# Kernel tuning notes

Measured on AMD Instinct MI355X. Metric: run time of the kernel, lower is better.

The kernel has to match this reference:

```python
import jax, jax.numpy as jnp
import numpy as np

# Config matching init_kwargs / input_specs
B, H, S, D = 4, 16, 4096, 64
BLK = 16          # sparsity_block
W = 32            # num_local_blocks (banded causal layout: block i attends blocks i-W+1..i)


def setup_inputs() -> dict:
    key = jax.random.key(0)
    kq, kk, kv = jax.random.split(key, 3)
    query = jax.random.normal(kq, (B, H, S, D), dtype=jnp.float16)
    k = jax.random.normal(kk, (B, H, S, D), dtype=jnp.float16)
    value = jax.random.normal(kv, (B, H, S, D), dtype=jnp.float16)
    return {"query": query, "key": k, "value": value}


def reference(query, key, value):
    b, h, s, d = query.shape
    nb = s // BLK
    scale = 1.0 / np.sqrt(d)

    qb = query.reshape(b, h, nb, BLK, d)
    kb = key.reshape(b, h, nb, BLK, d)
    vb = value.reshape(b, h, nb, BLK, d)

    # Banded causal block layout: for query block i, kv block indices i-W+1 .. i
    i = jnp.arange(nb)[:, None]                    # [nb,1]
    w = jnp.arange(W)[None, :]                     # [1,W]
    kv_idx = i - (W - 1) + w                       # [nb,W]
    valid = kv_idx >= 0
    idxc = jnp.clip(kv_idx, 0, nb - 1)

    kg = kb[:, :, idxc]                            # [B,H,nb,W,BLK,D] gathered K blocks
    vg = vb[:, :, idxc]                            # [B,H,nb,W,BLK,D]

    # SDD: block-sparse QK^T, only active blocks are computed
    scores = jnp.einsum('bhnqd,bhnwkd->bhnqwk', qb, kg).astype(jnp.float32) * scale

    # causal + validity mask on global token positions
    q_pos = (jnp.arange(nb) * BLK)[:, None, None, None] + jnp.arange(BLK)[None, :, None, None]  # [nb,BLK,1,1]
    k_pos = (kv_idx * BLK)[:, None, :, None] + jnp.arange(BLK)[None, None, None, :]             # [nb,1,W,BLK]
    mask = (k_pos <= q_pos) & valid[:, None, :, None]
    scores = jnp.where(mask, scores, -jnp.inf)

    # sparse softmax over all active key positions of each query row
    p = jax.nn.softmax(scores.reshape(b, h, nb, BLK, W * BLK), axis=-1)
    p = p.reshape(b, h, nb, BLK, W, BLK).astype(jnp.float16)

    # DSD: sparse-probabilities x dense-V
    out = jnp.einsum('bhnqwk,bhnwkd->bhnqd', p, vg)
    return out.reshape(b, h, s, d)
```

## Files before the change

kernel.cpp:

```cpp
#include <hip/hip_runtime.h>

#define SS 4096
#define DD 64
#define WW 32
#define NEG (-1e30f)
#define CSCALE 0.1803368801f

typedef _Float16 half8_t __attribute__((ext_vector_type(8)));
typedef __fp16 fp16x2_t __attribute__((ext_vector_type(2)));
typedef float float4_t __attribute__((ext_vector_type(4)));

static __device__ __forceinline__ unsigned pk(float a, float b) {
  fp16x2_t h = __builtin_amdgcn_cvt_pkrtz(a, b);
  return __builtin_bit_cast(unsigned, h);
}

static __device__ __forceinline__ half8_t cvt8s(const float* p, float c) {
  float4_t a = *(const float4_t*)p;
  float4_t b = *(const float4_t*)(p + 4);
  union { half8_t h; unsigned u[4]; } x;
  x.u[0] = pk(a[0] * c, a[1] * c);
  x.u[1] = pk(a[2] * c, a[3] * c);
  x.u[2] = pk(b[0] * c, b[1] * c);
  x.u[3] = pk(b[2] * c, b[3] * c);
  return x.h;
}

static __device__ __forceinline__ half8_t lds_frag16(const unsigned short* p) {
  union { half8_t h; uint4 u; } x;
  x.u = *(const uint4*)p;
  return x.h;
}

static __device__ __forceinline__ int ksig(int r) {
  return ((r & 3) ^ ((r >> 3) & 3)) | ((r & 2) << 1);
}

__global__ __launch_bounds__(256, 2)
void sparse_attn_kernel(const float* __restrict__ Q,
                        const float* __restrict__ K,
                        const float* __restrict__ V,
                        float* __restrict__ O) {
  extern __shared__ __align__(16) unsigned short smem[];
  unsigned short* kl = smem;
  unsigned short* vq = smem + 2 * 4096;

  const int lin = blockIdx.x;
  const int xcd = lin & 7;
  const int logical = (lin >> 3) + xcd * ((int)gridDim.x >> 3);
  const int bh = logical >> 5;
  const int i0 = (logical & 31) * 8;

  const int tid = threadIdx.x;
  const int wave = tid >> 6;
  const int lane = tid & 63;
  const int t = lane & 15;
  const int q = lane >> 4;

  const size_t base = (size_t)bh * SS * DD;
  const float* Qb = Q + base;
  const float* Kb = K + base;
  const float* Vb = V + base;

  const int iA = i0 + 2 * wave;
  const int iB = iA + 1;

  const float* qrowA = Qb + (size_t)(iA * 16 + t) * DD;
  const half8_t qfA0 = cvt8s(qrowA + q * 8, CSCALE);
  const half8_t qfA1 = cvt8s(qrowA + 32 + q * 8, CSCALE);
  const float* qrowB = Qb + (size_t)(iB * 16 + t) * DD;
  const half8_t qfB0 = cvt8s(qrowB + q * 8, CSCALE);
  const half8_t qfB1 = cvt8s(qrowB + 32 + q * 8, CSCALE);

  const int prow0 = ((t >> 2) << 3) + (t & 3);
  int koff[2][2];
#pragma unroll
  for (int p = 0; p < 2; ++p)
#pragma unroll
    for (int ro = 0; ro < 2; ++ro) {
      const int rowb = p * 32 + prow0 + ro * 4;
      koff[p][ro] = rowb * 64 + ((q ^ ksig(rowb)) << 3);
    }
  const int voff0 = t * 64 + (((q ^ (t >> 1)) & 7) << 3);

  float4_t accA[4], accB[4];
#pragma unroll
  for (int c = 0; c < 4; ++c) {
    accA[c] = {0.f, 0.f, 0.f, 0.f};
    accB[c] = {0.f, 0.f, 0.f, 0.f};
  }
  float lA = 0.0f, lB = 0.0f;

  const int lo_blk = (i0 - (WW - 1)) > 0 ? (i0 - (WW - 1)) : 0;
  const int Ulo = lo_blk >> 2;
  const int Uhi = (i0 + 7) >> 2;
  const int nit = Uhi - Ulo + 1;

  const int kr_ = tid >> 2;
  const int kcg = tid & 3;
  const int kst0 = kr_ * 64 + ((((kcg * 2) ^ ksig(kr_)) & 7) << 3);
  const int kst1 = kr_ * 64 + ((((kcg * 2 + 1) ^ ksig(kr_)) & 7) << 3);

  const int vdl = tid & 31;
  const int vg8 = (tid >> 5) & 7;
  const int vst0 = (2 * vdl) * 64 + (((vg8 ^ vdl) & 7) << 3);

  const float* kg = Kb + (size_t)(Ulo * 64 + kr_) * DD + kcg * 16;
  const float* vg = Vb + (size_t)(Ulo * 64 + vg8 * 8) * DD + vdl * 2;

  float4_t kv[4];
  float2 vv[8];

  auto load_raw = [&]() {
#pragma unroll
    for (int ii = 0; ii < 4; ++ii) kv[ii] = *(const float4_t*)(kg + ii * 4);
#pragma unroll
    for (int rr = 0; rr < 8; ++rr) vv[rr] = *(const float2*)(vg + rr * DD);
    kg += 64 * DD;
    vg += 64 * DD;
  };

  auto store_stage = [&](int bf) {
    uint4 w0, w1;
    w0.x = pk(kv[0][0], kv[0][1]);
    w0.y = pk(kv[0][2], kv[0][3]);
    w0.z = pk(kv[1][0], kv[1][1]);
    w0.w = pk(kv[1][2], kv[1][3]);
    w1.x = pk(kv[2][0], kv[2][1]);
    w1.y = pk(kv[2][2], kv[2][3]);
    w1.z = pk(kv[3][0], kv[3][1]);
    w1.w = pk(kv[3][2], kv[3][3]);
    unsigned short* kd = kl + bf * 4096;
    *(uint4*)(kd + kst0) = w0;
    *(uint4*)(kd + kst1) = w1;
    uint4 wlo, whi;
    wlo.x = pk(vv[0].x, vv[1].x);
    wlo.y = pk(vv[2].x, vv[3].x);
    wlo.z = pk(vv[4].x, vv[5].x);
    wlo.w = pk(vv[6].x, vv[7].x);
    whi.x = pk(vv[0].y, vv[1].y);
    whi.y = pk(vv[2].y, vv[3].y);
    whi.z = pk(vv[4].y, vv[5].y);
    whi.w = pk(vv[6].y, vv[7].y);
    unsigned short* vd = vq + bf * 4096 + vst0;
    *(uint4*)vd = wlo;
    *(uint4*)(vd + 64) = whi;
  };

  load_raw();

  for (int it = 0; it < nit; ++it) {
    const int U = Ulo + it;
    const int bf = it & 1;
    store_stage(bf);
    __syncthreads();
    if (it + 1 < nit) load_raw();

    const int U4 = 4 * U;
    if (U4 <= iB && U4 >= iA - 34) {
      const unsigned short* kd = kl + bf * 4096;
      float4_t stA[4], stB[4];
#pragma unroll
      for (int g = 0; g < 4; ++g) {
        stA[g] = {0.f, 0.f, 0.f, 0.f};
        stB[g] = {0.f, 0.f, 0.f, 0.f};
      }
#pragma unroll
      for (int p = 0; p < 2; ++p)
#pragma unroll
        for (int ro = 0; ro < 2; ++ro) {
          half8_t kf0 = lds_frag16(&kd[koff[p][ro]]);
          half8_t kf1 = lds_frag16(&kd[koff[p][ro] ^ 32]);
          const int g = p * 2 + ro;
          stA[g] = __builtin_amdgcn_mfma_f32_16x16x32_f16(kf0, qfA0, stA[g], 0, 0, 0);
          stA[g] = __builtin_amdgcn_mfma_f32_16x16x32_f16(kf1, qfA1, stA[g], 0, 0, 0);
          stB[g] = __builtin_amdgcn_mfma_f32_16x16x32_f16(kf0, qfB0, stB[g], 0, 0, 0);
          stB[g] = __builtin_amdgcn_mfma_f32_16x16x32_f16(kf1, qfB1, stB[g], 0, 0, 0);
        }

      float sA[4][4], sB[4][4];
      if (U4 >= iA - 30 && U4 + 3 < iA) {
#pragma unroll
        for (int g = 0; g < 4; ++g)
#pragma unroll
          for (int r = 0; r < 4; ++r) {
            sA[g][r] = stA[g][r];
            sB[g][r] = stB[g][r];
          }
      } else {
#pragma unroll
        for (int p = 0; p < 2; ++p) {
          const int jj = U4 + 2 * p + (q >> 1);
          const int kr = (q & 1) << 3;
#pragma unroll
          for (int ro = 0; ro < 2; ++ro)
#pragma unroll
            for (int r = 0; r < 4; ++r) {
              const int g = p * 2 + ro;
              float vA = stA[g][r], vB = stB[g][r];
              const bool dgm = (kr + ro * 4 + r > t);
              if ((jj < iA - (WW - 1)) || (jj > iA) || (jj == iA && dgm)) vA = NEG;
              if ((jj < iB - (WW - 1)) || (jj > iB) || (jj == iB && dgm)) vB = NEG;
              sA[g][r] = vA;
              sB[g][r] = vB;
            }
        }
      }

#pragma unroll
      for (int g = 0; g < 4; ++g)
#pragma unroll
        for (int r = 0; r < 4; ++r) {
          sA[g][r] = __builtin_exp2f(sA[g][r]);
          lA += sA[g][r];
          sB[g][r] = __builtin_exp2f(sB[g][r]);
          lB += sB[g][r];
        }

      union { half8_t h; unsigned u[4]; } pA0, pA1, pB0, pB1;
      pA0.u[0] = pk(sA[0][0], sA[0][1]);
      pA0.u[1] = pk(sA[0][2], sA[0][3]);
      pA0.u[2] = pk(sA[1][0], sA[1][1]);
      pA0.u[3] = pk(sA[1][2], sA[1][3]);
      pA1.u[0] = pk(sA[2][0], sA[2][1]);
      pA1.u[1] = pk(sA[2][2], sA[2][3]);
      pA1.u[2] = pk(sA[3][0], sA[3][1]);
      pA1.u[3] = pk(sA[3][2], sA[3][3]);
      pB0.u[0] = pk(sB[0][0], sB[0][1]);
      pB0.u[1] = pk(sB[0][2], sB[0][3]);
      pB0.u[2] = pk(sB[1][0], sB[1][1]);
      pB0.u[3] = pk(sB[1][2], sB[1][3]);
      pB1.u[0] = pk(sB[2][0], sB[2][1]);
      pB1.u[1] = pk(sB[2][2], sB[2][3]);
      pB1.u[2] = pk(sB[3][0], sB[3][1]);
      pB1.u[3] = pk(sB[3][2], sB[3][3]);

      const unsigned short* vd = vq + bf * 4096;
#pragma unroll
      for (int c = 0; c < 4; ++c) {
        const int vo = c * 1024 + voff0;
        half8_t va0 = lds_frag16(&vd[vo]);
        half8_t va1 = lds_frag16(&vd[vo ^ 32]);
        accA[c] = __builtin_amdgcn_mfma_f32_16x16x32_f16(va0, pA0.h, accA[c], 0, 0, 0);
        accA[c] = __builtin_amdgcn_mfma_f32_16x16x32_f16(va1, pA1.h, accA[c], 0, 0, 0);
        accB[c] = __builtin_amdgcn_mfma_f32_16x16x32_f16(va0, pB0.h, accB[c], 0, 0, 0);
        accB[c] = __builtin_amdgcn_mfma_f32_16x16x32_f16(va1, pB1.h, accB[c], 0, 0, 0);
      }
    }
  }

  float lAr = lA;
  lAr += __shfl_xor(lAr, 16);
  lAr += __shfl_xor(lAr, 32);
  const float invA = 1.0f / lAr;
  float* orowA = O + base + (size_t)(iA * 16 + t) * DD;
#pragma unroll
  for (int c = 0; c < 4; ++c) {
    float4_t ov;
#pragma unroll
    for (int r = 0; r < 4; ++r) ov[r] = accA[c][r] * invA;
    *(float4_t*)(orowA + c * 16 + q * 4) = ov;
  }
  float lBr = lB;
  lBr += __shfl_xor(lBr, 16);
  lBr += __shfl_xor(lBr, 32);
  const float invB = 1.0f / lBr;
  float* orowB = O + base + (size_t)(iB * 16 + t) * DD;
#pragma unroll
  for (int c = 0; c < 4; ++c) {
    float4_t ov;
#pragma unroll
    for (int r = 0; r < 4; ++r) ov[r] = accB[c][r] * invB;
    *(float4_t*)(orowB + c * 16 + q * 4) = ov;
  }
}

extern "C" void kernel_launch(void* const* d_in, const int* in_sizes, int n_in,
                              void* d_out, int out_size, void* d_ws, size_t ws_size,
                              hipStream_t stream) {
  const float* Q = (const float*)d_in[0];
  const float* K = (const float*)d_in[1];
  const float* V = (const float*)d_in[2];
  float* O = (float*)d_out;
  sparse_attn_kernel<<<dim3(2048), dim3(256), 65536, stream>>>(Q, K, V, O);
}
```

Measured before the change: 252.4 us.

## Pre-convert K/V to fp16 workspace and read fragments directly from global memory

```diff
diff --git a/kernel.cpp b/kernel.cpp
--- a/kernel.cpp
+++ b/kernel.cpp
@@ -26,7 +26,7 @@
   return x.h;
 }
 
-static __device__ __forceinline__ half8_t lds_frag16(const unsigned short* p) {
+static __device__ __forceinline__ half8_t frag16(const unsigned short* p) {
   union { half8_t h; uint4 u; } x;
   x.u = *(const uint4*)p;
   return x.h;
@@ -36,15 +36,67 @@
   return ((r & 3) ^ ((r >> 3) & 3)) | ((r & 2) << 1);
 }
 
-__global__ __launch_bounds__(256, 2)
-void sparse_attn_kernel(const float* __restrict__ Q,
-                        const float* __restrict__ K,
-                        const float* __restrict__ V,
+__global__ __launch_bounds__(256)
+void convert_kv(const float* __restrict__ K, const float* __restrict__ V,
+                unsigned short* __restrict__ K16,
+                unsigned short* __restrict__ V16t) {
+  const int blk = blockIdx.x;
+  const int bh = blk >> 6;
+  const int U = blk & 63;
+  const int tid = threadIdx.x;
+
+  const float* Kq = K + ((size_t)bh * SS + U * 64) * DD;
+  unsigned short* K16q = K16 + ((size_t)bh * SS + U * 64) * DD;
+#pragma unroll
+  for (int k2 = 0; k2 < 2; ++k2) {
+    const int u = k2 * 256 + tid;
+    const float* s = Kq + u * 8;
+    float4_t a = *(const float4_t*)s;
+    float4_t b = *(const float4_t*)(s + 4);
+    uint4 w;
+    w.x = pk(a[0], a[1]);
+    w.y = pk(a[2], a[3]);
+    w.z = pk(b[0], b[1]);
+    w.w = pk(b[2], b[3]);
+    *(uint4*)(K16q + u * 8) = w;
+  }
+
+  __shared__ __align__(16) unsigned short vt[64 * 64];
+  const int vdl = tid & 31;
+  const int vg8 = (tid >> 5) & 7;
+  const int vst0 = (2 * vdl) * 64 + (((vg8 ^ vdl) & 7) << 3);
+  const float* Vq = V + ((size_t)bh * SS + U * 64) * DD;
+  float2 vv[8];
+#pragma unroll
+  for (int rr = 0; rr < 8; ++rr)
+    vv[rr] = *(const float2*)(Vq + (size_t)(vg8 * 8 + rr) * DD + vdl * 2);
+  uint4 wlo, whi;
+  wlo.x = pk(vv[0].x, vv[1].x);
+  wlo.y = pk(vv[2].x, vv[3].x);
+  wlo.z = pk(vv[4].x, vv[5].x);
+  wlo.w = pk(vv[6].x, vv[7].x);
+  whi.x = pk(vv[0].y, vv[1].y);
+  whi.y = pk(vv[2].y, vv[3].y);
+  whi.z = pk(vv[4].y, vv[5].y);
+  whi.w = pk(vv[6].y, vv[7].y);
+  *(uint4*)&vt[vst0] = wlo;
+  *(uint4*)&vt[vst0 + 64] = whi;
+  __syncthreads();
+  const int d = tid >> 2;
+  const int c4 = tid & 3;
+  const int sg = (d >> 1) & 7;
+  uint4 lo = *(const uint4*)&vt[d * 64 + (((c4 * 2) ^ sg) << 3)];
+  uint4 hi = *(const uint4*)&vt[d * 64 + (((c4 * 2 + 1) ^ sg) << 3)];
+  unsigned short* dst = V16t + ((size_t)bh * DD + d) * SS + U * 64 + c4 * 16;
+  *(uint4*)dst = lo;
+  *(uint4*)(dst + 8) = hi;
+}
+
+__global__ __launch_bounds__(256, 3)
+void sparse_attn_direct(const float* __restrict__ Q,
+                        const unsigned short* __restrict__ K16,
+                        const unsigned short* __restrict__ V16t,
                         float* __restrict__ O) {
-  extern __shared__ __align__(16) unsigned short smem[];
-  unsigned short* kl = smem;
-  unsigned short* vq = smem + 2 * 4096;
-
   const int lin = blockIdx.x;
   const int xcd = lin & 7;
   const int logical = (lin >> 3) + xcd * ((int)gridDim.x >> 3);
@@ -59,8 +111,8 @@
 
   const size_t base = (size_t)bh * SS * DD;
   const float* Qb = Q + base;
-  const float* Kb = K + base;
-  const float* Vb = V + base;
+  const unsigned short* Kb = K16 + base;
+  const unsigned short* Vb = V16t + base;
 
   const int iA = i0 + 2 * wave;
   const int iB = iA + 1;
@@ -73,6 +125,181 @@
   const half8_t qfB1 = cvt8s(qrowB + 32 + q * 8, CSCALE);
 
   const int prow0 = ((t >> 2) << 3) + (t & 3);
+  int krow[2][2];
+#pragma unroll
+  for (int p = 0; p < 2; ++p)
+#pragma unroll
+    for (int ro = 0; ro < 2; ++ro)
+      krow[p][ro] = (p * 32 + prow0 + ro * 4) * DD + q * 8;
+  const int vcol = t * SS + q * 8;
+
+  float4_t accA[4], accB[4];
+#pragma unroll
+  for (int c = 0; c < 4; ++c) {
+    accA[c] = {0.f, 0.f, 0.f, 0.f};
+    accB[c] = {0.f, 0.f, 0.f, 0.f};
+  }
+  float lA = 0.0f, lB = 0.0f;
+
+  const int lo = (iA - (WW - 1)) > 0 ? (iA - (WW - 1)) : 0;
+  const int Ulo = lo >> 2;
+  const int Uhi = iB >> 2;
+
+  for (int U = Ulo; U <= Uhi; ++U) {
+    const int U4 = 4 * U;
+    const unsigned short* kq = Kb + (size_t)U * (64 * DD);
+
+    float4_t stA[4], stB[4];
+#pragma unroll
+    for (int g = 0; g < 4; ++g) {
+      stA[g] = {0.f, 0.f, 0.f, 0.f};
+      stB[g] = {0.f, 0.f, 0.f, 0.f};
+    }
+#pragma unroll
+    for (int p = 0; p < 2; ++p)
+#pragma unroll
+      for (int ro = 0; ro < 2; ++ro) {
+        half8_t kf0 = frag16(&kq[krow[p][ro]]);
+        half8_t kf1 = frag16(&kq[krow[p][ro] + 32]);
+        const int g = p * 2 + ro;
+        stA[g] = __builtin_amdgcn_mfma_f32_16x16x32_f16(kf0, qfA0, stA[g], 0, 0, 0);
+        stA[g] = __builtin_amdgcn_mfma_f32_16x16x32_f16(kf1, qfA1, stA[g], 0, 0, 0);
+        stB[g] = __builtin_amdgcn_mfma_f32_16x16x32_f16(kf0, qfB0, stB[g], 0, 0, 0);
+        stB[g] = __builtin_amdgcn_mfma_f32_16x16x32_f16(kf1, qfB1, stB[g], 0, 0, 0);
+      }
+
+    const unsigned short* vq_ = Vb + U * 64;
+    half8_t va0[4], va1[4];
+#pragma unroll
+    for (int c = 0; c < 4; ++c) {
+      const unsigned short* vp = &vq_[vcol + c * 16 * SS];
+      va0[c] = frag16(vp);
+      va1[c] = frag16(vp + 32);
+    }
+
+    float sA[4][4], sB[4][4];
+    if (U4 >= iA - 30 && U4 + 3 < iA) {
+#pragma unroll
+      for (int g = 0; g < 4; ++g)
+#pragma unroll
+        for (int r = 0; r < 4; ++r) {
+          sA[g][r] = stA[g][r];
+          sB[g][r] = stB[g][r];
+        }
+    } else {
+#pragma unroll
+      for (int p = 0; p < 2; ++p) {
+        const int jj = U4 + 2 * p + (q >> 1);
+        const int kr = (q & 1) << 3;
+#pragma unroll
+        for (int ro = 0; ro < 2; ++ro)
+#pragma unroll
+          for (int r = 0; r < 4; ++r) {
+            const int g = p * 2 + ro;
+            float vA = stA[g][r], vB = stB[g][r];
+            const bool dgm = (kr + ro * 4 + r > t);
+            if ((jj < iA - (WW - 1)) || (jj > iA) || (jj == iA && dgm)) vA = NEG;
+            if ((jj < iB - (WW - 1)) || (jj > iB) || (jj == iB && dgm)) vB = NEG;
+            sA[g][r] = vA;
+            sB[g][r] = vB;
+          }
+      }
+    }
+
+#pragma unroll
+    for (int g = 0; g < 4; ++g)
+#pragma unroll
+      for (int r = 0; r < 4; ++r) {
+        sA[g][r] = __builtin_exp2f(sA[g][r]);
+        lA += sA[g][r];
+        sB[g][r] = __builtin_exp2f(sB[g][r]);
+        lB += sB[g][r];
+      }
+
+    union { half8_t h; unsigned u[4]; } pA0, pA1, pB0, pB1;
+    pA0.u[0] = pk(sA[0][0], sA[0][1]);
+    pA0.u[1] = pk(sA[0][2], sA[0][3]);
+    pA0.u[2] = pk(sA[1][0], sA[1][1]);
+    pA0.u[3] = pk(sA[1][2], sA[1][3]);
+    pA1.u[0] = pk(sA[2][0], sA[2][1]);
+    pA1.u[1] = pk(sA[2][2], sA[2][3]);
+    pA1.u[2] = pk(sA[3][0], sA[3][1]);
+    pA1.u[3] = pk(sA[3][2], sA[3][3]);
+    pB0.u[0] = pk(sB[0][0], sB[0][1]);
+    pB0.u[1] = pk(sB[0][2], sB[0][3]);
+    pB0.u[2] = pk(sB[1][0], sB[1][1]);
+    pB0.u[3] = pk(sB[1][2], sB[1][3]);
+    pB1.u[0] = pk(sB[2][0], sB[2][1]);
+    pB1.u[1] = pk(sB[2][2], sB[2][3]);
+    pB1.u[2] = pk(sB[3][0], sB[3][1]);
+    pB1.u[3] = pk(sB[3][2], sB[3][3]);
+
+#pragma unroll
+    for (int c = 0; c < 4; ++c) {
+      accA[c] = __builtin_amdgcn_mfma_f32_16x16x32_f16(va0[c], pA0.h, accA[c], 0, 0, 0);
+      accA[c] = __builtin_amdgcn_mfma_f32_16x16x32_f16(va1[c], pA1.h, accA[c], 0, 0, 0);
+      accB[c] = __builtin_amdgcn_mfma_f32_16x16x32_f16(va0[c], pB0.h, accB[c], 0, 0, 0);
+      accB[c] = __builtin_amdgcn_mfma_f32_16x16x32_f16(va1[c], pB1.h, accB[c], 0, 0, 0);
+    }
+  }
+
+  float lAr = lA;
+  lAr += __shfl_xor(lAr, 16);
+  lAr += __shfl_xor(lAr, 32);
+  const float invA = 1.0f / lAr;
+  float* orowA = O + base + (size_t)(iA * 16 + t) * DD;
+#pragma unroll
+  for (int c = 0; c < 4; ++c) {
+    float4_t ov;
+#pragma unroll
+    for (int r = 0; r < 4; ++r) ov[r] = accA[c][r] * invA;
+    *(float4_t*)(orowA + c * 16 + q * 4) = ov;
+  }
+  float lBr = lB;
+  lBr += __shfl_xor(lBr, 16);
+  lBr += __shfl_xor(lBr, 32);
+  const float invB = 1.0f / lBr;
+  float* orowB = O + base + (size_t)(iB * 16 + t) * DD;
+#pragma unroll
+  for (int c = 0; c < 4; ++c) {
+    float4_t ov;
+#pragma unroll
+    for (int r = 0; r < 4; ++r) ov[r] = accB[c][r] * invB;
+    *(float4_t*)(orowB + c * 16 + q * 4) = ov;
+  }
+}
+
+__global__ __launch_bounds__(256, 2)
+void sparse_attn_fallback(const float* __restrict__ Q,
+                          const float* __restrict__ K,
+                          const float* __restrict__ V,
+                          float* __restrict__ O) {
+  extern __shared__ __align__(16) unsigned short smem[];
+  unsigned short* kl = smem;
+  unsigned short* vq = smem + 2 * 4096;
+  const int lin = blockIdx.x;
+  const int xcd = lin & 7;
+  const int logical = (lin >> 3) + xcd * ((int)gridDim.x >> 3);
+  const int bh = logical >> 5;
+  const int i0 = (logical & 31) * 8;
+  const int tid = threadIdx.x;
+  const int wave = tid >> 6;
+  const int lane = tid & 63;
+  const int t = lane & 15;
+  const int q = lane >> 4;
+  const size_t base = (size_t)bh * SS * DD;
+  const float* Qb = Q + base;
+  const float* Kb = K + base;
+  const float* Vb = V + base;
+  const int iA = i0 + 2 * wave;
+  const int iB = iA + 1;
+  const float* qrowA = Qb + (size_t)(iA * 16 + t) * DD;
+  const half8_t qfA0 = cvt8s(qrowA + q * 8, CSCALE);
+  const half8_t qfA1 = cvt8s(qrowA + 32 + q * 8, CSCALE);
+  const float* qrowB = Qb + (size_t)(iB * 16 + t) * DD;
+  const half8_t qfB0 = cvt8s(qrowB + q * 8, CSCALE);
+  const half8_t qfB1 = cvt8s(qrowB + 32 + q * 8, CSCALE);
+  const int prow0 = ((t >> 2) << 3) + (t & 3);
   int koff[2][2];
 #pragma unroll
   for (int p = 0; p < 2; ++p)
@@ -82,7 +309,6 @@
       koff[p][ro] = rowb * 64 + ((q ^ ksig(rowb)) << 3);
     }
   const int voff0 = t * 64 + (((q ^ (t >> 1)) & 7) << 3);
-
   float4_t accA[4], accB[4];
 #pragma unroll
   for (int c = 0; c < 4; ++c) {
@@ -90,27 +316,21 @@
     accB[c] = {0.f, 0.f, 0.f, 0.f};
   }
   float lA = 0.0f, lB = 0.0f;
-
   const int lo_blk = (i0 - (WW - 1)) > 0 ? (i0 - (WW - 1)) : 0;
   const int Ulo = lo_blk >> 2;
   const int Uhi = (i0 + 7) >> 2;
   const int nit = Uhi - Ulo + 1;
-
   const int kr_ = tid >> 2;
   const int kcg = tid & 3;
   const int kst0 = kr_ * 64 + ((((kcg * 2) ^ ksig(kr_)) & 7) << 3);
   const int kst1 = kr_ * 64 + ((((kcg * 2 + 1) ^ ksig(kr_)) & 7) << 3);
-
   const int vdl = tid & 31;
   const int vg8 = (tid >> 5) & 7;
   const int vst0 = (2 * vdl) * 64 + (((vg8 ^ vdl) & 7) << 3);
-
   const float* kg = Kb + (size_t)(Ulo * 64 + kr_) * DD + kcg * 16;
   const float* vg = Vb + (size_t)(Ulo * 64 + vg8 * 8) * DD + vdl * 2;
-
   float4_t kv[4];
   float2 vv[8];
-
   auto load_raw = [&]() {
 #pragma unroll
     for (int ii = 0; ii < 4; ++ii) kv[ii] = *(const float4_t*)(kg + ii * 4);
@@ -119,7 +339,6 @@
     kg += 64 * DD;
     vg += 64 * DD;
   };
-
   auto store_stage = [&](int bf) {
     uint4 w0, w1;
     w0.x = pk(kv[0][0], kv[0][1]);
@@ -146,16 +365,13 @@
     *(uint4*)vd = wlo;
     *(uint4*)(vd + 64) = whi;
   };
-
   load_raw();
-
   for (int it = 0; it < nit; ++it) {
     const int U = Ulo + it;
     const int bf = it & 1;
     store_stage(bf);
     __syncthreads();
     if (it + 1 < nit) load_raw();
-
     const int U4 = 4 * U;
     if (U4 <= iB && U4 >= iA - 34) {
       const unsigned short* kd = kl + bf * 4096;
@@ -169,15 +385,14 @@
       for (int p = 0; p < 2; ++p)
 #pragma unroll
         for (int ro = 0; ro < 2; ++ro) {
-          half8_t kf0 = lds_frag16(&kd[koff[p][ro]]);
-          half8_t kf1 = lds_frag16(&kd[koff[p][ro] ^ 32]);
+          half8_t kf0 = frag16(&kd[koff[p][ro]]);
+          half8_t kf1 = frag16(&kd[koff[p][ro] ^ 32]);
           const int g = p * 2 + ro;
           stA[g] = __builtin_amdgcn_mfma_f32_16x16x32_f16(kf0, qfA0, stA[g], 0, 0, 0);
           stA[g] = __builtin_amdgcn_mfma_f32_16x16x32_f16(kf1, qfA1, stA[g], 0, 0, 0);
           stB[g] = __builtin_amdgcn_mfma_f32_16x16x32_f16(kf0, qfB0, stB[g], 0, 0, 0);
           stB[g] = __builtin_amdgcn_mfma_f32_16x16x32_f16(kf1, qfB1, stB[g], 0, 0, 0);
         }
-
       float sA[4][4], sB[4][4];
       if (U4 >= iA - 30 && U4 + 3 < iA) {
 #pragma unroll
@@ -206,7 +421,6 @@
             }
         }
       }
-
 #pragma unroll
       for (int g = 0; g < 4; ++g)
 #pragma unroll
@@ -216,7 +430,6 @@
           sB[g][r] = __builtin_exp2f(sB[g][r]);
           lB += sB[g][r];
         }
-
       union { half8_t h; unsigned u[4]; } pA0, pA1, pB0, pB1;
       pA0.u[0] = pk(sA[0][0], sA[0][1]);
       pA0.u[1] = pk(sA[0][2], sA[0][3]);
@@ -234,13 +447,12 @@
       pB1.u[1] = pk(sB[2][2], sB[2][3]);
       pB1.u[2] = pk(sB[3][0], sB[3][1]);
       pB1.u[3] = pk(sB[3][2], sB[3][3]);
-
       const unsigned short* vd = vq + bf * 4096;
 #pragma unroll
       for (int c = 0; c < 4; ++c) {
         const int vo = c * 1024 + voff0;
-        half8_t va0 = lds_frag16(&vd[vo]);
-        half8_t va1 = lds_frag16(&vd[vo ^ 32]);
+        half8_t va0 = frag16(&vd[vo]);
+        half8_t va1 = frag16(&vd[vo ^ 32]);
         accA[c] = __builtin_amdgcn_mfma_f32_16x16x32_f16(va0, pA0.h, accA[c], 0, 0, 0);
         accA[c] = __builtin_amdgcn_mfma_f32_16x16x32_f16(va1, pA1.h, accA[c], 0, 0, 0);
         accB[c] = __builtin_amdgcn_mfma_f32_16x16x32_f16(va0, pB0.h, accB[c], 0, 0, 0);
@@ -248,7 +460,6 @@
       }
     }
   }
-
   float lAr = lA;
   lAr += __shfl_xor(lAr, 16);
   lAr += __shfl_xor(lAr, 32);
@@ -282,5 +493,13 @@
   const float* K = (const float*)d_in[1];
   const float* V = (const float*)d_in[2];
   float* O = (float*)d_out;
-  sparse_attn_kernel<<<dim3(2048), dim3(256), 65536, stream>>>(Q, K, V, O);
-}
+  const size_t kbytes = (size_t)64 * SS * DD * 2;
+  if (d_ws != nullptr && ws_size >= 2 * kbytes) {
+    unsigned short* K16 = (unsigned short*)d_ws;
+    unsigned short* V16t = (unsigned short*)((char*)d_ws + kbytes);
+    convert_kv<<<dim3(4096), dim3(256), 0, stream>>>(K, V, K16, V16t);
+    sparse_attn_direct<<<dim3(2048), dim3(256), 0, stream>>>(Q, K16, V16t, O);
+  } else {
+    sparse_attn_fallback<<<dim3(2048), dim3(256), 65536, stream>>>(Q, K, V, O);
+  }
+}
```

Result: slower. 356.8 us (+41.4%).
